# Kernel tuning notes

Measured on AMD Instinct MI355X. Metric: run time of the kernel, lower is better.

Reference implementation:

```python
import jax, jax.numpy as jnp
import numpy as np

N = 200_000            # nodes
E = 4_000_000          # edges
GCN_DIMS = [1, 20, 15, 12, 10]
NN_DIMS = [10, 32, 16, 8]
RAW = 16


def setup_inputs() -> dict:
    key = jax.random.key(0)
    ks = jax.random.split(key, 32)
    inp = {
        "x": jax.random.normal(ks[0], (N, GCN_DIMS[0]), dtype=jnp.float32),
        "edge_index": jax.random.randint(ks[1], (2, E), 0, N, dtype=jnp.int64),
    }
    ki = 2
    # GraphConv params: lin_rel (W_rel, b_rel) applied to aggregated neighbors,
    # lin_root (W_root, no bias) applied to self features.
    for i in range(4):
        fi, fo = GCN_DIMS[i], GCN_DIMS[i + 1]
        s = 1.0 / np.sqrt(fi)
        inp[f"gcn{i+1}_Wr"] = jax.random.uniform(ks[ki], (fo, fi), jnp.float32, -s, s); ki += 1
        inp[f"gcn{i+1}_b"]  = jax.random.uniform(ks[ki], (fo,),   jnp.float32, -s, s); ki += 1
        inp[f"gcn{i+1}_Wl"] = jax.random.uniform(ks[ki], (fo, fi), jnp.float32, -s, s); ki += 1
    fc_dims = NN_DIMS + [RAW]
    for i in range(4):
        fi, fo = fc_dims[i], fc_dims[i + 1]
        s = 1.0 / np.sqrt(fi)
        inp[f"fc{i+1}_W"] = jax.random.uniform(ks[ki], (fo, fi), jnp.float32, -s, s); ki += 1
        inp[f"fc{i+1}_b"] = jax.random.uniform(ks[ki], (fo,),   jnp.float32, -s, s); ki += 1
    return inp


def _graph_conv(x, src, tgt, deg_inv, Wr, b, Wl):
    # gather neighbor features, scatter-mean to targets, then two linears
    msg = x[src]                                            # [E, F]
    agg = jax.ops.segment_sum(msg, tgt, num_segments=N)     # [N, F]
    mean = agg * deg_inv                                    # [N, F]
    return mean @ Wr.T + b + x @ Wl.T                       # [N, Fo]


def reference(x, edge_index,
              gcn1_Wr, gcn1_b, gcn1_Wl, gcn2_Wr, gcn2_b, gcn2_Wl,
              gcn3_Wr, gcn3_b, gcn3_Wl, gcn4_Wr, gcn4_b, gcn4_Wl,
              fc1_W, fc1_b, fc2_W, fc2_b, fc3_W, fc3_b, fc4_W, fc4_b):
    sp = jax.nn.softplus
    src, tgt = edge_index[0], edge_index[1]
    cnt = jax.ops.segment_sum(jnp.ones((E,), x.dtype), tgt, num_segments=N)
    deg_inv = (1.0 / jnp.maximum(cnt, 1.0))[:, None]        # mean=0 for isolated nodes
    h = sp(_graph_conv(x, src, tgt, deg_inv, gcn1_Wr, gcn1_b, gcn1_Wl))
    h = sp(_graph_conv(h, src, tgt, deg_inv, gcn2_Wr, gcn2_b, gcn2_Wl))
    h = sp(_graph_conv(h, src, tgt, deg_inv, gcn3_Wr, gcn3_b, gcn3_Wl))
    h = sp(_graph_conv(h, src, tgt, deg_inv, gcn4_Wr, gcn4_b, gcn4_Wl))
    h = sp(h @ fc1_W.T + fc1_b)
    h = sp(h @ fc2_W.T + fc2_b)
    h = sp(h @ fc3_W.T + fc3_b)
    return h @ fc4_W.T + fc4_b
```

## Files before the change

### kernel.cpp

```cpp
#include <hip/hip_runtime.h>

#define NN 200000
#define NE 4000000

constexpr int BSH = 9;
constexpr int BW = 1 << BSH;
constexpr int NB2 = (NN + BW - 1) / BW;
constexpr int NWG1 = 512;
constexpr int CH = (NE + NWG1 - 1) / NWG1;
constexpr int CAP = 12288;
static_assert(NWG1 == 512, "shifts below assume 512");

__device__ __forceinline__ float softplus_f(float x) {
    return fmaxf(x, 0.0f) + log1pf(expf(-fabsf(x)));
}


__global__ __launch_bounds__(1024) void k_hist(const int* __restrict__ tgt,
                                               int* __restrict__ hist) {
    __shared__ int h[NB2];
    int w = blockIdx.x, t = threadIdx.x;
    for (int i = t; i < NB2; i += 1024) h[i] = 0;
    __syncthreads();
    int lo = w * CH, hi = min(lo + CH, NE);
    for (int e = lo + t; e < hi; e += 1024) atomicAdd(&h[tgt[e] >> BSH], 1);
    __syncthreads();
    for (int i = t; i < NB2; i += 1024) hist[w * NB2 + i] = h[i];
}

__global__ __launch_bounds__(512) void k_colscan(const int* __restrict__ hist,
                                                 int* __restrict__ loc,
                                                 int* __restrict__ bktot) {
    __shared__ int sd[512];
    int b = blockIdx.x, w = threadIdx.x;
    int v = hist[w * NB2 + b];
    sd[w] = v;
    __syncthreads();
    for (int off = 1; off < 512; off <<= 1) {
        int x = (w >= off) ? sd[w - off] : 0;
        __syncthreads();
        sd[w] += x;
        __syncthreads();
    }
    loc[b * NWG1 + w] = sd[w] - v;
    if (w == 511) bktot[b] = sd[511];
}

__global__ __launch_bounds__(512) void k_bktscan(const int* __restrict__ bktot,
                                                 int* __restrict__ bkbase) {
    __shared__ int sd[512];
    int t = threadIdx.x;
    int v = (t < NB2) ? bktot[t] : 0;
    sd[t] = v;
    __syncthreads();
    for (int off = 1; off < 512; off <<= 1) {
        int x = (t >= off) ? sd[t - off] : 0;
        __syncthreads();
        sd[t] += x;
        __syncthreads();
    }
    if (t < NB2) bkbase[t] = sd[t] - v;
    if (t == 0) bkbase[NB2] = NE;
}

__global__ __launch_bounds__(1024) void k_scatter(const int* __restrict__ ei,
                                                  const int* __restrict__ hist,
                                                  const int* __restrict__ loc,
                                                  const int* __restrict__ bkbase,
                                                  unsigned int* __restrict__ pair) {
    __shared__ int h[NB2], lc[NB2], adj[NB2];
    __shared__ int sc[512];
    __shared__ unsigned int stg[CH];
    __shared__ unsigned short stb[CH];
    int w = blockIdx.x, t = threadIdx.x;
    if (t < NB2) h[t] = hist[w * NB2 + t];
    if (t < 512) sc[t] = (t < NB2) ? hist[w * NB2 + t] : 0;
    __syncthreads();
    for (int off = 1; off < 512; off <<= 1) {
        int v = 0;
        if (t < 512 && t >= off) v = sc[t - off];
        __syncthreads();
        if (t < 512) sc[t] += v;
        __syncthreads();
    }
    if (t < NB2) {
        int lbase = sc[t] - h[t];
        lc[t] = lbase;
        adj[t] = loc[t * NWG1 + w] + bkbase[t] - lbase;
    }
    __syncthreads();
    int lo = w * CH, hi = min(lo + CH, NE);
    for (int e = lo + t; e < hi; e += 1024) {
        int s = ei[e], tg = ei[NE + e];
        int b = tg >> BSH;
        int lp = atomicAdd(&lc[b], 1);
        stg[lp] = ((unsigned int)s << BSH) | (unsigned int)(tg & (BW - 1));
        stb[lp] = (unsigned short)b;
    }
    __syncthreads();
    int n = hi - lo;
    for (int i = t; i < n; i += 1024) {
        pair[adj[stb[i]] + i] = stg[i];
    }
}

__global__ __launch_bounds__(1024) void k_bucketfill(const unsigned int* __restrict__ pair,
                                                     const int* __restrict__ bkbase,
                                                     int* __restrict__ rowptr,
                                                     float* __restrict__ dinv,
                                                     int* __restrict__ col) {
    __shared__ int nc[BW], sc[BW], cur[BW];
    __shared__ int colseg[CAP];
    int b = blockIdx.x, t = threadIdx.x;
    int lo = bkbase[b], hi = bkbase[b + 1];
    int cnt = hi - lo;
    if (t < BW) nc[t] = 0;
    __syncthreads();
    for (int e = lo + t; e < hi; e += 1024) atomicAdd(&nc[pair[e] & (BW - 1)], 1);
    __syncthreads();
    if (t < BW) sc[t] = nc[t];
    __syncthreads();
    for (int off = 1; off < BW; off <<= 1) {
        int v = 0;
        if (t < BW && t >= off) v = sc[t - off];
        __syncthreads();
        if (t < BW) sc[t] += v;
        __syncthreads();
    }
    if (t < BW) {
        int nofs = sc[t] - nc[t];
        cur[t] = nofs;
        int g = (b << BSH) + t;
        if (g < NN) {
            rowptr[g] = lo + nofs;
            dinv[g] = 1.0f / fmaxf((float)nc[t], 1.0f);
        }
    }
    if (b == NB2 - 1 && t == 0) rowptr[NN] = NE;
    __syncthreads();
    bool fast = (cnt <= CAP);
    for (int e = lo + t; e < hi; e += 1024) {
        unsigned int v = pair[e];
        int p = atomicAdd(&cur[v & (BW - 1)], 1);
        if (fast) colseg[p] = (int)(v >> BSH);
        else col[lo + p] = (int)(v >> BSH);
    }
    __syncthreads();
    if (fast) {
        for (int i = t; i < cnt; i += 1024) col[lo + i] = colseg[i];
    }
}


template <int FI, int LDI>
__device__ __forceinline__ void load_row(const float* __restrict__ p, float* v) {
    if constexpr (FI == 1) {
        v[0] = p[0];
        v[1] = 0.f; v[2] = 0.f; v[3] = 0.f;
    } else {
        constexpr int NV = (FI + 3) / 4;
        static_assert(NV * 4 <= LDI || FI == LDI, "row pad");
#pragma unroll
        for (int i = 0; i < NV; ++i) {
            float4 t = ((const float4*)p)[i];
            v[4 * i + 0] = t.x;
            v[4 * i + 1] = t.y;
            v[4 * i + 2] = t.z;
            v[4 * i + 3] = t.w;
        }
    }
}

template <int FI, int LDI>
__device__ __forceinline__ void gather_half(const float* __restrict__ xin,
                                            const int* __restrict__ col,
                                            int beg, int end, int half, float* s) {
    constexpr int NV = (FI + 3) / 4, RF = NV * 4;
#pragma unroll
    for (int f = 0; f < RF; ++f) s[f] = 0.f;
    int j = beg + half;
    for (; j + 2 < end; j += 4) {
        int c0 = __ldg(&col[j]);
        int c1 = __ldg(&col[j + 2]);
        float nv0[RF], nv1[RF];
        load_row<FI, LDI>(xin + (size_t)c0 * LDI, nv0);
        load_row<FI, LDI>(xin + (size_t)c1 * LDI, nv1);
#pragma unroll
        for (int f = 0; f < RF; ++f) s[f] += nv0[f] + nv1[f];
    }
    if (j < end) {
        int c = __ldg(&col[j]);
        float nv[RF];
        load_row<FI, LDI>(xin + (size_t)c * LDI, nv);
#pragma unroll
        for (int f = 0; f < RF; ++f) s[f] += nv[f];
    }
}

template <int FI, int LDI, int FO, int LDO>
__global__ __launch_bounds__(512, 6) void k_gcn(const float* __restrict__ xin,
                                                const int* __restrict__ rowptr,
                                                const int* __restrict__ col,
                                                const float* __restrict__ dinv,
                                                const float* __restrict__ Wr,
                                                const float* __restrict__ bias,
                                                const float* __restrict__ Wl,
                                                float* __restrict__ out) {
    constexpr int NV = (FI + 3) / 4, RF = NV * 4;
    constexpr int NVO = (FO + 3) / 4, RO = NVO * 4;
    static_assert(RO <= LDO, "out pad");
    __shared__ float sWr[FO * FI], sWl[FO * FI], sB[FO];
    for (int i = threadIdx.x; i < FO * FI; i += 512) {
        sWr[i] = Wr[i];
        sWl[i] = Wl[i];
    }
    if (threadIdx.x < FO) sB[threadIdx.x] = bias[threadIdx.x];
    __syncthreads();

    int t = threadIdx.x;
    int n = blockIdx.x * 256 + (t >> 1);
    int half = t & 1;
    if (n >= NN) return;

    float xv[RF];
    load_row<FI, LDI>(xin + (size_t)n * LDI, xv);

    int beg = rowptr[n], end = rowptr[n + 1];
    float s[RF];
    gather_half<FI, LDI>(xin, col, beg, end, half, s);
#pragma unroll
    for (int f = 0; f < RF; ++f) s[f] += __shfl_xor(s[f], 1);

    float di = dinv[n];
    float o_[RO];
#pragma unroll
    for (int o = 0; o < FO; ++o) {
        float aR = 0.f, aL = 0.f;
#pragma unroll
        for (int f = 0; f < FI; ++f) {
            aR = fmaf(s[f], sWr[o * FI + f], aR);
            aL = fmaf(xv[f], sWl[o * FI + f], aL);
        }
        o_[o] = softplus_f(fmaf(aR, di, sB[o]) + aL);
    }
#pragma unroll
    for (int o = FO; o < RO; ++o) o_[o] = 0.f;
    if (half == 0) {
#pragma unroll
        for (int i = 0; i < NVO; ++i) {
            ((float4*)(out + (size_t)n * LDO))[i] =
                make_float4(o_[4 * i], o_[4 * i + 1], o_[4 * i + 2], o_[4 * i + 3]);
        }
    }
}


__global__ __launch_bounds__(512, 6) void k_gcn4_fc(
    const float* __restrict__ xin,
    const int* __restrict__ rowptr, const int* __restrict__ col,
    const float* __restrict__ dinv, const float* __restrict__ Wr,
    const float* __restrict__ bias, const float* __restrict__ Wl,
    const float* __restrict__ f1W, const float* __restrict__ f1b,
    const float* __restrict__ f2W, const float* __restrict__ f2b,
    const float* __restrict__ f3W, const float* __restrict__ f3b,
    const float* __restrict__ f4W, const float* __restrict__ f4b,
    float* __restrict__ out)
{
    __shared__ float sWr[10 * 12], sWl[10 * 12], sB[10];
    __shared__ float s1W[32 * 10], s1b[32];
    __shared__ float s2W[16 * 32], s2b[16];
    __shared__ float s3W[8 * 16], s3b[8];
    __shared__ float s4W[16 * 8], s4b[16];
    for (int i = threadIdx.x; i < 120; i += 512) {
        sWr[i] = Wr[i];
        sWl[i] = Wl[i];
    }
    for (int i = threadIdx.x; i < 320; i += 512) s1W[i] = f1W[i];
    for (int i = threadIdx.x; i < 512; i += 512) s2W[i] = f2W[i];
    for (int i = threadIdx.x; i < 128; i += 512) s3W[i] = f3W[i];
    for (int i = threadIdx.x; i < 128; i += 512) s4W[i] = f4W[i];
    if (threadIdx.x < 10) sB[threadIdx.x] = bias[threadIdx.x];
    if (threadIdx.x < 32) s1b[threadIdx.x] = f1b[threadIdx.x];
    if (threadIdx.x < 16) s2b[threadIdx.x] = f2b[threadIdx.x];
    if (threadIdx.x < 8) s3b[threadIdx.x] = f3b[threadIdx.x];
    if (threadIdx.x < 16) s4b[threadIdx.x] = f4b[threadIdx.x];
    __syncthreads();

    int t = threadIdx.x;
    int n = blockIdx.x * 256 + (t >> 1);
    int half = t & 1;
    if (n >= NN) return;

    constexpr int FI = 12, LDI = 12;
    float xv[12];
    load_row<FI, LDI>(xin + (size_t)n * LDI, xv);
    int beg = rowptr[n], end = rowptr[n + 1];
    float s[12];
    gather_half<FI, LDI>(xin, col, beg, end, half, s);
#pragma unroll
    for (int f = 0; f < 12; ++f) s[f] += __shfl_xor(s[f], 1);
    float di = dinv[n];

    float a0[10];
#pragma unroll
    for (int o = 0; o < 10; ++o) {
        float aR = 0.f, aL = 0.f;
#pragma unroll
        for (int f = 0; f < 12; ++f) {
            aR = fmaf(s[f], sWr[o * 12 + f], aR);
            aL = fmaf(xv[f], sWl[o * 12 + f], aL);
        }
        a0[o] = softplus_f(fmaf(aR, di, sB[o]) + aL);
    }

    float a1[32];
#pragma unroll
    for (int o = 0; o < 32; ++o) {
        float acc = s1b[o];
#pragma unroll
        for (int f = 0; f < 10; ++f) acc = fmaf(a0[f], s1W[o * 10 + f], acc);
        a1[o] = softplus_f(acc);
    }
    float a2[16];
#pragma unroll
    for (int o = 0; o < 16; ++o) {
        float acc = s2b[o];
#pragma unroll
        for (int f = 0; f < 32; ++f) acc = fmaf(a1[f], s2W[o * 32 + f], acc);
        a2[o] = softplus_f(acc);
    }
    float a3[8];
#pragma unroll
    for (int o = 0; o < 8; ++o) {
        float acc = s3b[o];
#pragma unroll
        for (int f = 0; f < 16; ++f) acc = fmaf(a2[f], s3W[o * 16 + f], acc);
        a3[o] = softplus_f(acc);
    }
    float a4[16];
#pragma unroll
    for (int o = 0; o < 16; ++o) {
        float acc = s4b[o];
#pragma unroll
        for (int f = 0; f < 8; ++f) acc = fmaf(a3[f], s4W[o * 8 + f], acc);
        a4[o] = acc;
    }

    if (half == 0) {
        float4* po = (float4*)(out + (size_t)n * 16);
#pragma unroll
        for (int i = 0; i < 4; ++i)
            po[i] = make_float4(a4[4 * i], a4[4 * i + 1], a4[4 * i + 2], a4[4 * i + 3]);
    }
}


extern "C" void kernel_launch(void* const* d_in, const int* in_sizes, int n_in,
                              void* d_out, int out_size, void* d_ws, size_t ws_size,
                              hipStream_t stream) {
    const float* x = (const float*)d_in[0];
    const int* ei = (const int*)d_in[1];
    const float* g1Wr = (const float*)d_in[2];
    const float* g1b = (const float*)d_in[3];
    const float* g1Wl = (const float*)d_in[4];
    const float* g2Wr = (const float*)d_in[5];
    const float* g2b = (const float*)d_in[6];
    const float* g2Wl = (const float*)d_in[7];
    const float* g3Wr = (const float*)d_in[8];
    const float* g3b = (const float*)d_in[9];
    const float* g3Wl = (const float*)d_in[10];
    const float* g4Wr = (const float*)d_in[11];
    const float* g4b = (const float*)d_in[12];
    const float* g4Wl = (const float*)d_in[13];
    const float* f1W = (const float*)d_in[14];
    const float* f1b = (const float*)d_in[15];
    const float* f2W = (const float*)d_in[16];
    const float* f2b = (const float*)d_in[17];
    const float* f3W = (const float*)d_in[18];
    const float* f3b = (const float*)d_in[19];
    const float* f4W = (const float*)d_in[20];
    const float* f4b = (const float*)d_in[21];
    float* out = (float*)d_out;

    char* ws = (char*)d_ws;
    size_t off = 0;
    auto alloc = [&](size_t bytes) {
        void* p = ws + off;
        off = (off + bytes + 255) & ~(size_t)255;
        return p;
    };
    int* hist = (int*)alloc((size_t)NWG1 * NB2 * 4);
    int* loc = (int*)alloc((size_t)NB2 * NWG1 * 4);
    int* bktot = (int*)alloc((size_t)NB2 * 4);
    int* bkbase = (int*)alloc((size_t)(NB2 + 1) * 4);
    unsigned int* pair = (unsigned int*)alloc((size_t)NE * 4);
    int* rowptr = (int*)alloc((size_t)(NN + 1) * 4);
    float* dinv = (float*)alloc((size_t)NN * 4);
    int* col = (int*)alloc((size_t)NE * 4);
    float* hA = (float*)alloc((size_t)NN * 20 * 4);
    float* hB = out;

    k_hist<<<NWG1, 1024, 0, stream>>>(ei + NE, hist);
    k_colscan<<<NB2, 512, 0, stream>>>(hist, loc, bktot);
    k_bktscan<<<1, 512, 0, stream>>>(bktot, bkbase);
    k_scatter<<<NWG1, 1024, 0, stream>>>(ei, hist, loc, bkbase, pair);
    k_bucketfill<<<NB2, 1024, 0, stream>>>(pair, bkbase, rowptr, dinv, col);

    const int GB = (NN + 255) / 256;
    k_gcn<1, 1, 20, 20><<<GB, 512, 0, stream>>>(x, rowptr, col, dinv, g1Wr, g1b, g1Wl, hA);
    k_gcn<20, 20, 15, 16><<<GB, 512, 0, stream>>>(hA, rowptr, col, dinv, g2Wr, g2b, g2Wl, hB);
    k_gcn<15, 16, 12, 12><<<GB, 512, 0, stream>>>(hB, rowptr, col, dinv, g3Wr, g3b, g3Wl, hA);
    k_gcn4_fc<<<GB, 512, 0, stream>>>(hA, rowptr, col, dinv, g4Wr, g4b, g4Wl, f1W, f1b, f2W,
                                      f2b, f3W, f3b, f4W, f4b, out);
}
```

Baseline: 589.2 us.

## Transform features before aggregation so gathers use projected narrower rows

Uses linearity of mean aggregation: each layer now precomputes y = h·Wr^T and z = h·Wl^T + b per node, and the next kernel gathers y rows and applies softplus(mean(y) + z). Layer 2 therefore gathers 15-wide rows instead of 20-wide, and each layer's matmul runs once per node rather than after aggregation. All gathered rows are padded to 16 floats for float4 loads. In exchange, each layer writes and reads an extra z array, and scratch buffers are reused through the pair workspace.

```diff
diff --git a/kernel.cpp b/kernel.cpp
--- a/kernel.cpp
+++ b/kernel.cpp
@@ -152,69 +152,75 @@
 }
 
 
-template <int FI, int LDI>
-__device__ __forceinline__ void load_row(const float* __restrict__ p, float* v) {
-    if constexpr (FI == 1) {
-        v[0] = p[0];
-        v[1] = 0.f; v[2] = 0.f; v[3] = 0.f;
-    } else {
-        constexpr int NV = (FI + 3) / 4;
-        static_assert(NV * 4 <= LDI || FI == LDI, "row pad");
-#pragma unroll
-        for (int i = 0; i < NV; ++i) {
-            float4 t = ((const float4*)p)[i];
-            v[4 * i + 0] = t.x;
-            v[4 * i + 1] = t.y;
-            v[4 * i + 2] = t.z;
-            v[4 * i + 3] = t.w;
-        }
-    }
-}
-
-template <int FI, int LDI>
-__device__ __forceinline__ void gather_half(const float* __restrict__ xin,
-                                            const int* __restrict__ col,
-                                            int beg, int end, int half, float* s) {
-    constexpr int NV = (FI + 3) / 4, RF = NV * 4;
-#pragma unroll
-    for (int f = 0; f < RF; ++f) s[f] = 0.f;
+__global__ __launch_bounds__(512, 6) void k_gcn1(
+    const float* __restrict__ x, const int* __restrict__ rowptr,
+    const int* __restrict__ col, const float* __restrict__ dinv,
+    const float* __restrict__ Wr1, const float* __restrict__ b1,
+    const float* __restrict__ Wl1, const float* __restrict__ Wr2,
+    const float* __restrict__ b2, const float* __restrict__ Wl2,
+    float* __restrict__ y2, float* __restrict__ z2) {
+    __shared__ float sWr1[20], sB1[20], sWl1[20];
+    __shared__ float sWr2[15 * 20], sWl2[15 * 20], sB2[15];
+    int t = threadIdx.x;
+    if (t < 20) { sWr1[t] = Wr1[t]; sB1[t] = b1[t]; sWl1[t] = Wl1[t]; }
+    for (int i = t; i < 300; i += 512) { sWr2[i] = Wr2[i]; sWl2[i] = Wl2[i]; }
+    if (t < 15) sB2[t] = b2[t];
+    __syncthreads();
+
+    int n = blockIdx.x * 256 + (t >> 1);
+    int half = t & 1;
+    if (n >= NN) return;
+
+    float xn = x[n];
+    int beg = rowptr[n], end = rowptr[n + 1];
+    float s = 0.f;
     int j = beg + half;
     for (; j + 2 < end; j += 4) {
-        int c0 = __ldg(&col[j]);
-        int c1 = __ldg(&col[j + 2]);
-        float nv0[RF], nv1[RF];
-        load_row<FI, LDI>(xin + (size_t)c0 * LDI, nv0);
-        load_row<FI, LDI>(xin + (size_t)c1 * LDI, nv1);
-#pragma unroll
-        for (int f = 0; f < RF; ++f) s[f] += nv0[f] + nv1[f];
-    }
-    if (j < end) {
-        int c = __ldg(&col[j]);
-        float nv[RF];
-        load_row<FI, LDI>(xin + (size_t)c * LDI, nv);
-#pragma unroll
-        for (int f = 0; f < RF; ++f) s[f] += nv[f];
-    }
-}
-
-template <int FI, int LDI, int FO, int LDO>
-__global__ __launch_bounds__(512, 6) void k_gcn(const float* __restrict__ xin,
-                                                const int* __restrict__ rowptr,
-                                                const int* __restrict__ col,
-                                                const float* __restrict__ dinv,
-                                                const float* __restrict__ Wr,
-                                                const float* __restrict__ bias,
-                                                const float* __restrict__ Wl,
-                                                float* __restrict__ out) {
-    constexpr int NV = (FI + 3) / 4, RF = NV * 4;
-    constexpr int NVO = (FO + 3) / 4, RO = NVO * 4;
-    static_assert(RO <= LDO, "out pad");
-    __shared__ float sWr[FO * FI], sWl[FO * FI], sB[FO];
-    for (int i = threadIdx.x; i < FO * FI; i += 512) {
-        sWr[i] = Wr[i];
-        sWl[i] = Wl[i];
-    }
-    if (threadIdx.x < FO) sB[threadIdx.x] = bias[threadIdx.x];
+        int c0 = __ldg(&col[j]), c1 = __ldg(&col[j + 2]);
+        s += __ldg(&x[c0]) + __ldg(&x[c1]);
+    }
+    if (j < end) s += __ldg(&x[__ldg(&col[j])]);
+    s += __shfl_xor(s, 1);
+
+    if (half) return;
+    float mean = s * dinv[n];
+    float h1[20];
+#pragma unroll
+    for (int o = 0; o < 20; ++o)
+        h1[o] = softplus_f(fmaf(mean, sWr1[o], fmaf(xn, sWl1[o], sB1[o])));
+
+    float yo[16], zo[16];
+#pragma unroll
+    for (int o = 0; o < 15; ++o) {
+        float ay = 0.f, az = 0.f;
+#pragma unroll
+        for (int f = 0; f < 20; ++f) {
+            ay = fmaf(h1[f], sWr2[o * 20 + f], ay);
+            az = fmaf(h1[f], sWl2[o * 20 + f], az);
+        }
+        yo[o] = ay;
+        zo[o] = az + sB2[o];
+    }
+    yo[15] = 0.f; zo[15] = 0.f;
+    float4* py = (float4*)(y2 + (size_t)n * 16);
+    float4* pz = (float4*)(z2 + (size_t)n * 16);
+#pragma unroll
+    for (int i = 0; i < 4; ++i) {
+        py[i] = make_float4(yo[4 * i], yo[4 * i + 1], yo[4 * i + 2], yo[4 * i + 3]);
+        pz[i] = make_float4(zo[4 * i], zo[4 * i + 1], zo[4 * i + 2], zo[4 * i + 3]);
+    }
+}
+
+template <int FO, int NFO>
+__global__ __launch_bounds__(512, 6) void k_gcnT(
+    const float* __restrict__ yin, const float* __restrict__ zin,
+    const int* __restrict__ rowptr, const int* __restrict__ col,
+    const float* __restrict__ dinv, const float* __restrict__ WrN,
+    const float* __restrict__ bN, const float* __restrict__ WlN,
+    float* __restrict__ yout, float* __restrict__ zout) {
+    __shared__ float sWr[NFO * FO], sWl[NFO * FO], sB[NFO];
+    for (int i = threadIdx.x; i < NFO * FO; i += 512) { sWr[i] = WrN[i]; sWl[i] = WlN[i]; }
+    if (threadIdx.x < NFO) sB[threadIdx.x] = bN[threadIdx.x];
     __syncthreads();
 
     int t = threadIdx.x;
@@ -222,64 +228,91 @@
     int half = t & 1;
     if (n >= NN) return;
 
-    float xv[RF];
-    load_row<FI, LDI>(xin + (size_t)n * LDI, xv);
-
+    float s[16];
+#pragma unroll
+    for (int f = 0; f < 16; ++f) s[f] = 0.f;
     int beg = rowptr[n], end = rowptr[n + 1];
-    float s[RF];
-    gather_half<FI, LDI>(xin, col, beg, end, half, s);
-#pragma unroll
-    for (int f = 0; f < RF; ++f) s[f] += __shfl_xor(s[f], 1);
-
+    int j = beg + half;
+    for (; j + 2 < end; j += 4) {
+        int c0 = __ldg(&col[j]), c1 = __ldg(&col[j + 2]);
+        const float4* p0 = (const float4*)(yin + (size_t)c0 * 16);
+        const float4* p1 = (const float4*)(yin + (size_t)c1 * 16);
+        float4 v0[4], v1[4];
+#pragma unroll
+        for (int i = 0; i < 4; ++i) { v0[i] = p0[i]; v1[i] = p1[i]; }
+#pragma unroll
+        for (int i = 0; i < 4; ++i) {
+            s[4 * i + 0] += v0[i].x + v1[i].x;
+            s[4 * i + 1] += v0[i].y + v1[i].y;
+            s[4 * i + 2] += v0[i].z + v1[i].z;
+            s[4 * i + 3] += v0[i].w + v1[i].w;
+        }
+    }
+    if (j < end) {
+        const float4* p0 = (const float4*)(yin + (size_t)__ldg(&col[j]) * 16);
+#pragma unroll
+        for (int i = 0; i < 4; ++i) {
+            float4 v = p0[i];
+            s[4 * i + 0] += v.x; s[4 * i + 1] += v.y;
+            s[4 * i + 2] += v.z; s[4 * i + 3] += v.w;
+        }
+    }
+#pragma unroll
+    for (int f = 0; f < 16; ++f) s[f] += __shfl_xor(s[f], 1);
+
+    if (half) return;
     float di = dinv[n];
-    float o_[RO];
-#pragma unroll
-    for (int o = 0; o < FO; ++o) {
-        float aR = 0.f, aL = 0.f;
-#pragma unroll
-        for (int f = 0; f < FI; ++f) {
-            aR = fmaf(s[f], sWr[o * FI + f], aR);
-            aL = fmaf(xv[f], sWl[o * FI + f], aL);
-        }
-        o_[o] = softplus_f(fmaf(aR, di, sB[o]) + aL);
-    }
-#pragma unroll
-    for (int o = FO; o < RO; ++o) o_[o] = 0.f;
-    if (half == 0) {
-#pragma unroll
-        for (int i = 0; i < NVO; ++i) {
-            ((float4*)(out + (size_t)n * LDO))[i] =
-                make_float4(o_[4 * i], o_[4 * i + 1], o_[4 * i + 2], o_[4 * i + 3]);
-        }
-    }
-}
-
+    const float4* pzr = (const float4*)(zin + (size_t)n * 16);
+    float zr[16];
+#pragma unroll
+    for (int i = 0; i < 4; ++i) {
+        float4 v = pzr[i];
+        zr[4 * i] = v.x; zr[4 * i + 1] = v.y; zr[4 * i + 2] = v.z; zr[4 * i + 3] = v.w;
+    }
+    float h[FO];
+#pragma unroll
+    for (int f = 0; f < FO; ++f) h[f] = softplus_f(fmaf(s[f], di, zr[f]));
+
+    float yo[16], zo[16];
+#pragma unroll
+    for (int o = 0; o < NFO; ++o) {
+        float ay = 0.f, az = 0.f;
+#pragma unroll
+        for (int f = 0; f < FO; ++f) {
+            ay = fmaf(h[f], sWr[o * FO + f], ay);
+            az = fmaf(h[f], sWl[o * FO + f], az);
+        }
+        yo[o] = ay;
+        zo[o] = az + sB[o];
+    }
+#pragma unroll
+    for (int o = NFO; o < 16; ++o) { yo[o] = 0.f; zo[o] = 0.f; }
+    float4* py = (float4*)(yout + (size_t)n * 16);
+    float4* pz = (float4*)(zout + (size_t)n * 16);
+#pragma unroll
+    for (int i = 0; i < 4; ++i) {
+        py[i] = make_float4(yo[4 * i], yo[4 * i + 1], yo[4 * i + 2], yo[4 * i + 3]);
+        pz[i] = make_float4(zo[4 * i], zo[4 * i + 1], zo[4 * i + 2], zo[4 * i + 3]);
+    }
+}
 
 __global__ __launch_bounds__(512, 6) void k_gcn4_fc(
-    const float* __restrict__ xin,
+    const float* __restrict__ yin, const float* __restrict__ zin,
     const int* __restrict__ rowptr, const int* __restrict__ col,
-    const float* __restrict__ dinv, const float* __restrict__ Wr,
-    const float* __restrict__ bias, const float* __restrict__ Wl,
+    const float* __restrict__ dinv,
     const float* __restrict__ f1W, const float* __restrict__ f1b,
     const float* __restrict__ f2W, const float* __restrict__ f2b,
     const float* __restrict__ f3W, const float* __restrict__ f3b,
     const float* __restrict__ f4W, const float* __restrict__ f4b,
-    float* __restrict__ out)
-{
-    __shared__ float sWr[10 * 12], sWl[10 * 12], sB[10];
+    float* __restrict__ out) {
     __shared__ float s1W[32 * 10], s1b[32];
     __shared__ float s2W[16 * 32], s2b[16];
     __shared__ float s3W[8 * 16], s3b[8];
     __shared__ float s4W[16 * 8], s4b[16];
-    for (int i = threadIdx.x; i < 120; i += 512) {
-        sWr[i] = Wr[i];
-        sWl[i] = Wl[i];
-    }
     for (int i = threadIdx.x; i < 320; i += 512) s1W[i] = f1W[i];
     for (int i = threadIdx.x; i < 512; i += 512) s2W[i] = f2W[i];
     for (int i = threadIdx.x; i < 128; i += 512) s3W[i] = f3W[i];
     for (int i = threadIdx.x; i < 128; i += 512) s4W[i] = f4W[i];
-    if (threadIdx.x < 10) sB[threadIdx.x] = bias[threadIdx.x];
     if (threadIdx.x < 32) s1b[threadIdx.x] = f1b[threadIdx.x];
     if (threadIdx.x < 16) s2b[threadIdx.x] = f2b[threadIdx.x];
     if (threadIdx.x < 8) s3b[threadIdx.x] = f3b[threadIdx.x];
@@ -291,27 +324,50 @@
     int half = t & 1;
     if (n >= NN) return;
 
-    constexpr int FI = 12, LDI = 12;
-    float xv[12];
-    load_row<FI, LDI>(xin + (size_t)n * LDI, xv);
+    float s[16];
+#pragma unroll
+    for (int f = 0; f < 16; ++f) s[f] = 0.f;
     int beg = rowptr[n], end = rowptr[n + 1];
-    float s[12];
-    gather_half<FI, LDI>(xin, col, beg, end, half, s);
-#pragma unroll
-    for (int f = 0; f < 12; ++f) s[f] += __shfl_xor(s[f], 1);
+    int j = beg + half;
+    for (; j + 2 < end; j += 4) {
+        int c0 = __ldg(&col[j]), c1 = __ldg(&col[j + 2]);
+        const float4* p0 = (const float4*)(yin + (size_t)c0 * 16);
+        const float4* p1 = (const float4*)(yin + (size_t)c1 * 16);
+        float4 v0[4], v1[4];
+#pragma unroll
+        for (int i = 0; i < 4; ++i) { v0[i] = p0[i]; v1[i] = p1[i]; }
+#pragma unroll
+        for (int i = 0; i < 4; ++i) {
+            s[4 * i + 0] += v0[i].x + v1[i].x;
+            s[4 * i + 1] += v0[i].y + v1[i].y;
+            s[4 * i + 2] += v0[i].z + v1[i].z;
+            s[4 * i + 3] += v0[i].w + v1[i].w;
+        }
+    }
+    if (j < end) {
+        const float4* p0 = (const float4*)(yin + (size_t)__ldg(&col[j]) * 16);
+#pragma unroll
+        for (int i = 0; i < 4; ++i) {
+            float4 v = p0[i];
+            s[4 * i + 0] += v.x; s[4 * i + 1] += v.y;
+            s[4 * i + 2] += v.z; s[4 * i + 3] += v.w;
+        }
+    }
+#pragma unroll
+    for (int f = 0; f < 16; ++f) s[f] += __shfl_xor(s[f], 1);
+
+    if (half) return;
     float di = dinv[n];
-
+    const float4* pzr = (const float4*)(zin + (size_t)n * 16);
+    float zr[16];
+#pragma unroll
+    for (int i = 0; i < 4; ++i) {
+        float4 v = pzr[i];
+        zr[4 * i] = v.x; zr[4 * i + 1] = v.y; zr[4 * i + 2] = v.z; zr[4 * i + 3] = v.w;
+    }
     float a0[10];
 #pragma unroll
-    for (int o = 0; o < 10; ++o) {
-        float aR = 0.f, aL = 0.f;
-#pragma unroll
-        for (int f = 0; f < 12; ++f) {
-            aR = fmaf(s[f], sWr[o * 12 + f], aR);
-            aL = fmaf(xv[f], sWl[o * 12 + f], aL);
-        }
-        a0[o] = softplus_f(fmaf(aR, di, sB[o]) + aL);
-    }
+    for (int f = 0; f < 10; ++f) a0[f] = softplus_f(fmaf(s[f], di, zr[f]));
 
     float a1[32];
 #pragma unroll
@@ -345,13 +401,10 @@
         for (int f = 0; f < 8; ++f) acc = fmaf(a3[f], s4W[o * 8 + f], acc);
         a4[o] = acc;
     }
-
-    if (half == 0) {
-        float4* po = (float4*)(out + (size_t)n * 16);
-#pragma unroll
-        for (int i = 0; i < 4; ++i)
-            po[i] = make_float4(a4[4 * i], a4[4 * i + 1], a4[4 * i + 2], a4[4 * i + 3]);
-    }
+    float4* po = (float4*)(out + (size_t)n * 16);
+#pragma unroll
+    for (int i = 0; i < 4; ++i)
+        po[i] = make_float4(a4[4 * i], a4[4 * i + 1], a4[4 * i + 2], a4[4 * i + 3]);
 }
 
 
@@ -397,8 +450,12 @@
     int* rowptr = (int*)alloc((size_t)(NN + 1) * 4);
     float* dinv = (float*)alloc((size_t)NN * 4);
     int* col = (int*)alloc((size_t)NE * 4);
-    float* hA = (float*)alloc((size_t)NN * 20 * 4);
-    float* hB = out;
+    float* z2 = (float*)alloc((size_t)NN * 16 * 4);
+    float* y3 = (float*)alloc((size_t)NN * 16 * 4);
+    float* z3 = (float*)alloc((size_t)NN * 16 * 4);
+    float* y2 = (float*)pair;
+    float* y4 = (float*)pair;
+    float* z4 = z2;
 
     k_hist<<<NWG1, 1024, 0, stream>>>(ei + NE, hist);
     k_colscan<<<NB2, 512, 0, stream>>>(hist, loc, bktot);
@@ -407,9 +464,12 @@
     k_bucketfill<<<NB2, 1024, 0, stream>>>(pair, bkbase, rowptr, dinv, col);
 
     const int GB = (NN + 255) / 256;
-    k_gcn<1, 1, 20, 20><<<GB, 512, 0, stream>>>(x, rowptr, col, dinv, g1Wr, g1b, g1Wl, hA);
-    k_gcn<20, 20, 15, 16><<<GB, 512, 0, stream>>>(hA, rowptr, col, dinv, g2Wr, g2b, g2Wl, hB);
-    k_gcn<15, 16, 12, 12><<<GB, 512, 0, stream>>>(hB, rowptr, col, dinv, g3Wr, g3b, g3Wl, hA);
-    k_gcn4_fc<<<GB, 512, 0, stream>>>(hA, rowptr, col, dinv, g4Wr, g4b, g4Wl, f1W, f1b, f2W,
-                                      f2b, f3W, f3b, f4W, f4b, out);
-}
+    k_gcn1<<<GB, 512, 0, stream>>>(x, rowptr, col, dinv, g1Wr, g1b, g1Wl, g2Wr, g2b, g2Wl,
+                                   y2, z2);
+    k_gcnT<15, 12><<<GB, 512, 0, stream>>>(y2, z2, rowptr, col, dinv, g3Wr, g3b, g3Wl,
+                                           y3, z3);
+    k_gcnT<12, 10><<<GB, 512, 0, stream>>>(y3, z3, rowptr, col, dinv, g4Wr, g4b, g4Wl,
+                                           y4, z4);
+    k_gcn4_fc<<<GB, 512, 0, stream>>>(y4, z4, rowptr, col, dinv, f1W, f1b, f2W, f2b, f3W,
+                                      f3b, f4W, f4b, out);
+}
```

Result: faster. 551.6 us, median of 2 (-6.4%).
